# Kernel tuning notes

Measured on AMD Instinct MI355X. Metric: run time of the kernel, lower is better.

The kernel has to match this reference:

```python
import jax, jax.numpy as jnp
import numpy as np


def position_embedding(seq_len, d):
    # inv_freq_j = 1 / 10000^(2*j/d), pos_ij = sin(i * inv_freq_j)  -> [S, d]
    inv_freq = 1.0 / jnp.power(10000.0, 2.0 * jnp.arange(d, dtype=jnp.float32) / d)
    pos = jnp.arange(seq_len, dtype=jnp.float32)
    return jnp.sin(pos[:, None] * inv_freq[None, :])  # [S, d]


def setup_inputs() -> dict:
    key = jax.random.key(0)
    k1, k2 = jax.random.split(key)
    B, S, D, OUT = 4, 4096, 64, 64
    x = jax.random.normal(k1, (B, S, D), dtype=jnp.float32)
    kernel = jax.random.normal(k2, (3, D, OUT), dtype=jnp.float32) * 0.05
    return {"x": x, "kernel": kernel}


def reference(x, kernel):
    B, S, D = x.shape
    out_dim = kernel.shape[2]
    x = x + position_embedding(S, D)[None, :, :]  # broadcast pos-embed over batch
    # stacked QKV projection: [B,S,D] x [D,out] per slot
    wq = jnp.einsum('bsd,do->bso', x, kernel[0])
    wk = jnp.einsum('bsd,do->bso', x, kernel[1])
    wv = jnp.einsum('bsd,do->bso', x, kernel[2])
    scores = jnp.einsum('bso,bto->bst', wq, wk) / jnp.sqrt(jnp.asarray(out_dim, x.dtype))
    attn = jax.nn.softmax(scores, axis=-1)  # [B,S,S]
    return jnp.einsum('bst,bto->bso', attn, wv)
```

## Files before the change

### kernel.cpp

```cpp
#include <hip/hip_runtime.h>
#include <hip/hip_bf16.h>
#include <math.h>

using bf16x8 = __attribute__((ext_vector_type(8))) __bf16;
using bf16x4 = __attribute__((ext_vector_type(4))) __bf16;
using f32x4  = __attribute__((ext_vector_type(4))) float;
using f32x16 = __attribute__((ext_vector_type(16))) float;

static constexpr int SEQ = 4096;
static constexpr int DIM = 64;
static constexpr int NB  = 4;
static constexpr float QSCALE = 0.18033688011112042f;

__device__ __forceinline__ void gload16(const void* g, void* l) {
    __builtin_amdgcn_global_load_lds(
        (const __attribute__((address_space(1))) unsigned int*)g,
        (__attribute__((address_space(3))) unsigned int*)l,
        16, 0, 0);
}

__device__ __forceinline__ float fast_exp2(float x) {
#if __has_builtin(__builtin_amdgcn_exp2f)
    return __builtin_amdgcn_exp2f(x);
#else
    return exp2f(x);
#endif
}

__global__ __launch_bounds__(256)
void const_prep_kernel(const float* __restrict__ w, __bf16* __restrict__ WT,
                       float* __restrict__ peb)
{
    const int idx = (int)blockIdx.x * 256 + (int)threadIdx.x;
    const int spos = idx >> 6;
    const int c    = idx & 63;
    const float invf = exp2f(-13.287712379549449f * ((float)c * 0.03125f));
    peb[idx] = __sinf((float)spos * invf);
    if (idx < 3 * DIM * DIM) {
        const int s = idx >> 12;
        const int o = (idx >> 6) & 63;
        const int d = idx & 63;
        WT[idx] = (__bf16)w[(s * DIM + d) * DIM + o];
    }
}

__global__ __launch_bounds__(256)
void qkv_prep_kernel(const float* __restrict__ x, const __bf16* __restrict__ WT,
                     const float* __restrict__ peb,
                     __bf16* __restrict__ Qb, __bf16* __restrict__ Kb,
                     __bf16* __restrict__ Vf)
{
    const int tid  = (int)threadIdx.x;
    const int lane = tid & 63;
    const int g  = lane >> 4;
    const int cl = lane & 15;
    const int rowbase = (int)blockIdx.x * 64 + (tid >> 6) * 16;

    const int row  = rowbase + cl;
    const int spos = row & (SEQ - 1);
    bf16x8 xa[2];
#pragma unroll
    for (int h = 0; h < 2; ++h) {
        const float* xp = x + (long)row * DIM + 32*h + 8*g;
        const float* pp = peb + (long)spos * DIM + 32*h + 8*g;
        f32x4 x0 = *reinterpret_cast<const f32x4*>(xp);
        f32x4 x1 = *reinterpret_cast<const f32x4*>(xp + 4);
        f32x4 p0 = *reinterpret_cast<const f32x4*>(pp);
        f32x4 p1 = *reinterpret_cast<const f32x4*>(pp + 4);
        bf16x8 v;
#pragma unroll
        for (int e = 0; e < 8; ++e) {
            const float xv = (e < 4) ? x0[e] : x1[e - 4];
            const float pe = (e < 4) ? p0[e] : p1[e - 4];
            v[e] = (__bf16)(xv + pe);
        }
        xa[h] = v;
    }

#pragma unroll
    for (int slot = 0; slot < 3; ++slot) {
        const __bf16* wt = WT + slot * DIM * DIM;
        f32x4 acc[4];
#pragma unroll
        for (int nt = 0; nt < 4; ++nt) acc[nt] = (f32x4){0.f, 0.f, 0.f, 0.f};
#pragma unroll
        for (int nt = 0; nt < 4; ++nt) {
            bf16x8 w0 = *reinterpret_cast<const bf16x8*>(wt + (nt*16 + cl) * DIM + 8*g);
            bf16x8 w1 = *reinterpret_cast<const bf16x8*>(wt + (nt*16 + cl) * DIM + 32 + 8*g);
            acc[nt] = __builtin_amdgcn_mfma_f32_16x16x32_bf16(xa[0], w0, acc[nt], 0, 0, 0);
            acc[nt] = __builtin_amdgcn_mfma_f32_16x16x32_bf16(xa[1], w1, acc[nt], 0, 0, 0);
        }

        if (slot < 2) {
            __bf16* dst = (slot == 0) ? Qb : Kb;
            const float scale = (slot == 0) ? QSCALE : 1.0f;
#pragma unroll
            for (int nt = 0; nt < 4; ++nt)
#pragma unroll
                for (int r = 0; r < 4; ++r) {
                    const int ro = rowbase + 4*g + r;
                    dst[(long)ro * DIM + nt*16 + cl] = (__bf16)(acc[nt][r] * scale);
                }
        } else {
            const int bi = rowbase >> 12;
            const int sp = rowbase & (SEQ - 1);
            const int kc = sp >> 5;
            const int ks = (sp >> 4) & 1;
            const int lde = (32*(g&1) + cl)*8 + (g>>1)*4;
            __bf16* vb = Vf + (((long)bi*128 + kc)*4 + ks*2)*512;
#pragma unroll
            for (int nt = 0; nt < 4; ++nt) {
                bf16x4 pk;
#pragma unroll
                for (int r = 0; r < 4; ++r) pk[r] = (__bf16)acc[nt][r];
                *reinterpret_cast<bf16x4*>(vb + (nt>>1)*512 + (nt&1)*128 + lde) = pk;
            }
        }
    }
}

__global__ __launch_bounds__(512, 2)
void attn_kernel(const __bf16* __restrict__ Qb, const __bf16* __restrict__ Kb,
                 const __bf16* __restrict__ Vf, float* __restrict__ out)
{
    __shared__ char smem[71680];

    const int tid  = (int)threadIdx.x;
    const int w    = tid >> 6;
    const int lane = tid & 63;
    const int hi   = lane >> 5;
    const int l31  = lane & 31;

    const int bid = (int)blockIdx.x;
    const int x8  = bid & 7;
    const int b   = x8 & 3;
    const int qt  = ((x8 >> 2) << 6) | (bid >> 3);
    const int qbase = qt * 32;

    const __bf16* Qp  = Qb + ((long)b * SEQ + qbase) * DIM;
    const __bf16* Kpw = Kb + ((long)b * SEQ + w * 512) * DIM;
    const __bf16* Vfp = Vf + (((long)b * 128 + w * 16) * 4) * 512;

    bf16x8 qf[4];
#pragma unroll
    for (int d4 = 0; d4 < 4; ++d4)
        qf[d4] = *reinterpret_cast<const bf16x8*>(Qp + l31*DIM + d4*16 + 8*hi);

    char* kbase = smem + w * 8192;
    const int srow = lane >> 3;
    const int ssw  = ((lane & 7) ^ srow) * 8;
    int rdo[4];
#pragma unroll
    for (int d4 = 0; d4 < 4; ++d4)
        rdo[d4] = l31*128 + (((2*d4 + hi) ^ (l31 & 7)) * 16);

    f32x16 acc[2];
#pragma unroll
    for (int dt = 0; dt < 2; ++dt)
#pragma unroll
        for (int r = 0; r < 16; ++r) acc[dt][r] = 0.f;
    float mrun = -INFINITY;
    float lsum = 0.f;

    bf16x8 vcur[4], vnxt[4];
#pragma unroll
    for (int j = 0; j < 4; ++j)
        gload16(Kpw + (long)(j*8 + srow) * DIM + ssw, kbase + j*1024 + lane*16);
#pragma unroll
    for (int f = 0; f < 4; ++f)
        vcur[f] = *reinterpret_cast<const bf16x8*>(Vfp + f*512 + lane*8);

#pragma unroll 2
    for (int n = 0; n < 16; ++n) {
        if (n < 15) {
            const __bf16* kp = Kpw + (long)((n + 1) * 32) * DIM;
            char* kdst = kbase + ((n & 1) ^ 1) * 4096;
#pragma unroll
            for (int j = 0; j < 4; ++j)
                gload16(kp + (long)(j*8 + srow) * DIM + ssw, kdst + j*1024 + lane*16);
            const __bf16* vp = Vfp + (long)(n + 1) * 2048;
#pragma unroll
            for (int f = 0; f < 4; ++f)
                vnxt[f] = *reinterpret_cast<const bf16x8*>(vp + f*512 + lane*8);
            asm volatile("s_waitcnt vmcnt(8)" ::: "memory");
        } else {
            asm volatile("s_waitcnt vmcnt(0)" ::: "memory");
        }
        __builtin_amdgcn_sched_barrier(0);

        const char* kb = kbase + (n & 1) * 4096;
        bf16x8 kf0 = *reinterpret_cast<const bf16x8*>(kb + rdo[0]);
        bf16x8 kf1 = *reinterpret_cast<const bf16x8*>(kb + rdo[1]);
        bf16x8 kf2 = *reinterpret_cast<const bf16x8*>(kb + rdo[2]);
        bf16x8 kf3 = *reinterpret_cast<const bf16x8*>(kb + rdo[3]);
        f32x16 s;
#pragma unroll
        for (int r = 0; r < 16; ++r) s[r] = 0.f;
        __builtin_amdgcn_s_setprio(1);
        s = __builtin_amdgcn_mfma_f32_32x32x16_bf16(kf0, qf[0], s, 0, 0, 0);
        s = __builtin_amdgcn_mfma_f32_32x32x16_bf16(kf1, qf[1], s, 0, 0, 0);
        s = __builtin_amdgcn_mfma_f32_32x32x16_bf16(kf2, qf[2], s, 0, 0, 0);
        s = __builtin_amdgcn_mfma_f32_32x32x16_bf16(kf3, qf[3], s, 0, 0, 0);
        __builtin_amdgcn_s_setprio(0);

        float tmax = fmaxf(fmaxf(s[0], s[1]), fmaxf(s[2], s[3]));
        tmax = fmaxf(tmax, fmaxf(fmaxf(s[4], s[5]), fmaxf(s[6], s[7])));
        tmax = fmaxf(tmax, fmaxf(fmaxf(s[8], s[9]), fmaxf(s[10], s[11])));
        tmax = fmaxf(tmax, fmaxf(fmaxf(s[12], s[13]), fmaxf(s[14], s[15])));
        tmax = fmaxf(tmax, __shfl_xor(tmax, 32));

        if (!__all(tmax <= mrun)) {
            const float mnew = fmaxf(mrun, tmax);
            const float corr = fast_exp2(mrun - mnew);
            lsum *= corr;
#pragma unroll
            for (int r = 0; r < 16; ++r) {
                acc[0][r] *= corr;
                acc[1][r] *= corr;
            }
            mrun = mnew;
        }

#pragma unroll
        for (int r = 0; r < 16; ++r) {
            const float p = fast_exp2(s[r] - mrun);
            s[r] = p;
            lsum += p;
        }

        bf16x8 pb0, pb1;
#pragma unroll
        for (int e = 0; e < 8; ++e) { pb0[e] = (__bf16)s[e]; pb1[e] = (__bf16)s[8 + e]; }

        __builtin_amdgcn_s_setprio(1);
        acc[0] = __builtin_amdgcn_mfma_f32_32x32x16_bf16(vcur[0], pb0, acc[0], 0, 0, 0);
        acc[1] = __builtin_amdgcn_mfma_f32_32x32x16_bf16(vcur[1], pb0, acc[1], 0, 0, 0);
        acc[0] = __builtin_amdgcn_mfma_f32_32x32x16_bf16(vcur[2], pb1, acc[0], 0, 0, 0);
        acc[1] = __builtin_amdgcn_mfma_f32_32x32x16_bf16(vcur[3], pb1, acc[1], 0, 0, 0);
        __builtin_amdgcn_s_setprio(0);

#pragma unroll
        for (int f = 0; f < 4; ++f) vcur[f] = vnxt[f];
    }

    lsum += __shfl_xor(lsum, 32);

    __syncthreads();
    float* lpart = (float*)smem;
    float* lm    = (float*)(smem + 69632);
    float* ll    = (float*)(smem + 70656);

    {
        float* lw = lpart + ((long)w*32 + l31) * 68;
#pragma unroll
        for (int dt = 0; dt < 2; ++dt)
#pragma unroll
            for (int j = 0; j < 4; ++j) {
                f32x4 v;
#pragma unroll
                for (int c = 0; c < 4; ++c) v[c] = acc[dt][4*j + c];
                *reinterpret_cast<f32x4*>(lw + dt*32 + 8*j + 4*hi) = v;
            }
        if (lane < 32) { lm[w*32 + l31] = mrun; ll[w*32 + l31] = lsum; }
    }
    __syncthreads();

    {
        const int q  = tid >> 4;
        const int dq = (tid & 15) * 4;
        float M = lm[q];
#pragma unroll
        for (int w2 = 1; w2 < 8; ++w2) M = fmaxf(M, lm[w2*32 + q]);
        float L = 0.f;
        f32x4 o = (f32x4){0.f, 0.f, 0.f, 0.f};
#pragma unroll
        for (int w2 = 0; w2 < 8; ++w2) {
            const float f = fast_exp2(lm[w2*32 + q] - M);
            L += ll[w2*32 + q] * f;
            f32x4 v = *reinterpret_cast<const f32x4*>(lpart + ((long)w2*32 + q)*68 + dq);
#pragma unroll
            for (int c = 0; c < 4; ++c) o[c] += v[c] * f;
        }
        const float inv = 1.f / L;
#pragma unroll
        for (int c = 0; c < 4; ++c) o[c] *= inv;
        *reinterpret_cast<f32x4*>(out + ((long)b * SEQ + qbase + q) * DIM + dq) = o;
    }
}

extern "C" void kernel_launch(void* const* d_in, const int* in_sizes, int n_in,
                              void* d_out, int out_size, void* d_ws, size_t ws_size,
                              hipStream_t stream)
{
    const float* x = (const float*)d_in[0];
    const float* w = (const float*)d_in[1];
    float* out = (float*)d_out;

    char* ws = (char*)d_ws;
    const size_t sz = (size_t)NB * SEQ * DIM * sizeof(__bf16);
    __bf16* Qb  = (__bf16*)(ws);
    __bf16* Kb  = (__bf16*)(ws + sz);
    __bf16* Vf  = (__bf16*)(ws + 2 * sz);
    __bf16* WT  = (__bf16*)(ws + 3 * sz);
    float*  peb = (float*)(ws + 3 * sz + 32 * 1024);

    const_prep_kernel<<<SEQ * DIM / 256, 256, 0, stream>>>(w, WT, peb);

    qkv_prep_kernel<<<NB * SEQ / 64, 256, 0, stream>>>(x, WT, peb, Qb, Kb, Vf);

    attn_kernel<<<NB * SEQ / 32, 512, 0, stream>>>(Qb, Kb, Vf, out);
}
```

Measured before the change: 52.67 us.

## Store Q/K in MFMA fragment layout, load K directly to registers, tree-merge partials

The QKV prep kernel now writes Q and K pre-swizzled into the per-lane MFMA fragment layout, so the attention kernel loads K straight into registers with coalesced 16-byte loads instead of staging it through LDS with async global_load_lds. V is now loaded at the start of each iteration rather than prefetched one step ahead. The cross-wave softmax merge becomes a pairwise tree reduction, which roughly halves LDS use and drops the occupancy hint from launch bounds. The aim is to remove LDS traffic and waitcnt stalls and allow more occupancy, at the risk of exposing V load latency and adding extra barriers in the reduction.

```diff
diff --git a/kernel.cpp b/kernel.cpp
--- a/kernel.cpp
+++ b/kernel.cpp
@@ -11,13 +11,6 @@
 static constexpr int DIM = 64;
 static constexpr int NB  = 4;
 static constexpr float QSCALE = 0.18033688011112042f;
-
-__device__ __forceinline__ void gload16(const void* g, void* l) {
-    __builtin_amdgcn_global_load_lds(
-        (const __attribute__((address_space(1))) unsigned int*)g,
-        (__attribute__((address_space(3))) unsigned int*)l,
-        16, 0, 0);
-}
 
 __device__ __forceinline__ float fast_exp2(float x) {
 #if __has_builtin(__builtin_amdgcn_exp2f)
@@ -47,7 +40,7 @@
 __global__ __launch_bounds__(256)
 void qkv_prep_kernel(const float* __restrict__ x, const __bf16* __restrict__ WT,
                      const float* __restrict__ peb,
-                     __bf16* __restrict__ Qb, __bf16* __restrict__ Kb,
+                     __bf16* __restrict__ Qf, __bf16* __restrict__ Kf,
                      __bf16* __restrict__ Vf)
 {
     const int tid  = (int)threadIdx.x;
@@ -77,6 +70,11 @@
         xa[h] = v;
     }
 
+    const int bi  = rowbase >> 12;
+    const int sp  = rowbase & (SEQ - 1);
+    const int c32 = sp >> 5;
+    const int rb16 = sp & 16;
+
 #pragma unroll
     for (int slot = 0; slot < 3; ++slot) {
         const __bf16* wt = WT + slot * DIM * DIM;
@@ -87,31 +85,35 @@
         for (int nt = 0; nt < 4; ++nt) {
             bf16x8 w0 = *reinterpret_cast<const bf16x8*>(wt + (nt*16 + cl) * DIM + 8*g);
             bf16x8 w1 = *reinterpret_cast<const bf16x8*>(wt + (nt*16 + cl) * DIM + 32 + 8*g);
-            acc[nt] = __builtin_amdgcn_mfma_f32_16x16x32_bf16(xa[0], w0, acc[nt], 0, 0, 0);
-            acc[nt] = __builtin_amdgcn_mfma_f32_16x16x32_bf16(xa[1], w1, acc[nt], 0, 0, 0);
+            if (slot < 2) {
+                acc[nt] = __builtin_amdgcn_mfma_f32_16x16x32_bf16(w0, xa[0], acc[nt], 0, 0, 0);
+                acc[nt] = __builtin_amdgcn_mfma_f32_16x16x32_bf16(w1, xa[1], acc[nt], 0, 0, 0);
+            } else {
+                acc[nt] = __builtin_amdgcn_mfma_f32_16x16x32_bf16(xa[0], w0, acc[nt], 0, 0, 0);
+                acc[nt] = __builtin_amdgcn_mfma_f32_16x16x32_bf16(xa[1], w1, acc[nt], 0, 0, 0);
+            }
         }
 
         if (slot < 2) {
-            __bf16* dst = (slot == 0) ? Qb : Kb;
+            __bf16* dst = (slot == 0) ? Qf : Kf;
             const float scale = (slot == 0) ? QSCALE : 1.0f;
-#pragma unroll
-            for (int nt = 0; nt < 4; ++nt)
-#pragma unroll
-                for (int r = 0; r < 4; ++r) {
-                    const int ro = rowbase + 4*g + r;
-                    dst[(long)ro * DIM + nt*16 + cl] = (__bf16)(acc[nt][r] * scale);
-                }
-        } else {
-            const int bi = rowbase >> 12;
-            const int sp = rowbase & (SEQ - 1);
-            const int kc = sp >> 5;
-            const int ks = (sp >> 4) & 1;
-            const int lde = (32*(g&1) + cl)*8 + (g>>1)*4;
-            __bf16* vb = Vf + (((long)bi*128 + kc)*4 + ks*2)*512;
+            __bf16* base = dst + ((long)(bi*128 + c32) * 4) * 512
+                         + (rb16 + cl + 32*(g >> 1)) * 8 + 4*(g & 1);
 #pragma unroll
             for (int nt = 0; nt < 4; ++nt) {
                 bf16x4 pk;
 #pragma unroll
+                for (int r = 0; r < 4; ++r) pk[r] = (__bf16)(acc[nt][r] * scale);
+                *reinterpret_cast<bf16x4*>(base + nt*512) = pk;
+            }
+        } else {
+            const int ks  = (sp >> 4) & 1;
+            const int lde = (32*(g&1) + cl)*8 + (g>>1)*4;
+            __bf16* vb = Vf + (((long)bi*128 + c32)*4 + ks*2)*512;
+#pragma unroll
+            for (int nt = 0; nt < 4; ++nt) {
+                bf16x4 pk;
+#pragma unroll
                 for (int r = 0; r < 4; ++r) pk[r] = (__bf16)acc[nt][r];
                 *reinterpret_cast<bf16x4*>(vb + (nt>>1)*512 + (nt&1)*128 + lde) = pk;
             }
@@ -119,11 +121,14 @@
     }
 }
 
-__global__ __launch_bounds__(512, 2)
-void attn_kernel(const __bf16* __restrict__ Qb, const __bf16* __restrict__ Kb,
+__global__ __launch_bounds__(512)
+void attn_kernel(const __bf16* __restrict__ Qf, const __bf16* __restrict__ Kf,
                  const __bf16* __restrict__ Vf, float* __restrict__ out)
 {
-    __shared__ char smem[71680];
+    __shared__ char smem[35840];
+    float* lpart = (float*)smem;
+    float* lms   = (float*)(smem + 34816);
+    float* lls   = (float*)(smem + 35328);
 
     const int tid  = (int)threadIdx.x;
     const int w    = tid >> 6;
@@ -137,22 +142,14 @@
     const int qt  = ((x8 >> 2) << 6) | (bid >> 3);
     const int qbase = qt * 32;
 
-    const __bf16* Qp  = Qb + ((long)b * SEQ + qbase) * DIM;
-    const __bf16* Kpw = Kb + ((long)b * SEQ + w * 512) * DIM;
-    const __bf16* Vfp = Vf + (((long)b * 128 + w * 16) * 4) * 512;
+    const __bf16* Qfp = Qf + ((long)(b*128 + qt)  * 4) * 512 + lane*8;
+    const __bf16* Kfp = Kf + ((long)(b*128 + w*16) * 4) * 512 + lane*8;
+    const __bf16* Vfp = Vf + ((long)(b*128 + w*16) * 4) * 512 + lane*8;
 
     bf16x8 qf[4];
 #pragma unroll
     for (int d4 = 0; d4 < 4; ++d4)
-        qf[d4] = *reinterpret_cast<const bf16x8*>(Qp + l31*DIM + d4*16 + 8*hi);
-
-    char* kbase = smem + w * 8192;
-    const int srow = lane >> 3;
-    const int ssw  = ((lane & 7) ^ srow) * 8;
-    int rdo[4];
-#pragma unroll
-    for (int d4 = 0; d4 < 4; ++d4)
-        rdo[d4] = l31*128 + (((2*d4 + hi) ^ (l31 & 7)) * 16);
+        qf[d4] = *reinterpret_cast<const bf16x8*>(Qfp + d4*512);
 
     f32x16 acc[2];
 #pragma unroll
@@ -162,45 +159,30 @@
     float mrun = -INFINITY;
     float lsum = 0.f;
 
-    bf16x8 vcur[4], vnxt[4];
-#pragma unroll
-    for (int j = 0; j < 4; ++j)
-        gload16(Kpw + (long)(j*8 + srow) * DIM + ssw, kbase + j*1024 + lane*16);
-#pragma unroll
-    for (int f = 0; f < 4; ++f)
-        vcur[f] = *reinterpret_cast<const bf16x8*>(Vfp + f*512 + lane*8);
+    bf16x8 kcur[4], knxt[4], vcur[4];
+#pragma unroll
+    for (int d4 = 0; d4 < 4; ++d4)
+        kcur[d4] = *reinterpret_cast<const bf16x8*>(Kfp + d4*512);
 
 #pragma unroll 2
     for (int n = 0; n < 16; ++n) {
+#pragma unroll
+        for (int f = 0; f < 4; ++f)
+            vcur[f] = *reinterpret_cast<const bf16x8*>(Vfp + n*2048 + f*512);
         if (n < 15) {
-            const __bf16* kp = Kpw + (long)((n + 1) * 32) * DIM;
-            char* kdst = kbase + ((n & 1) ^ 1) * 4096;
-#pragma unroll
-            for (int j = 0; j < 4; ++j)
-                gload16(kp + (long)(j*8 + srow) * DIM + ssw, kdst + j*1024 + lane*16);
-            const __bf16* vp = Vfp + (long)(n + 1) * 2048;
-#pragma unroll
-            for (int f = 0; f < 4; ++f)
-                vnxt[f] = *reinterpret_cast<const bf16x8*>(vp + f*512 + lane*8);
-            asm volatile("s_waitcnt vmcnt(8)" ::: "memory");
-        } else {
-            asm volatile("s_waitcnt vmcnt(0)" ::: "memory");
-        }
-        __builtin_amdgcn_sched_barrier(0);
-
-        const char* kb = kbase + (n & 1) * 4096;
-        bf16x8 kf0 = *reinterpret_cast<const bf16x8*>(kb + rdo[0]);
-        bf16x8 kf1 = *reinterpret_cast<const bf16x8*>(kb + rdo[1]);
-        bf16x8 kf2 = *reinterpret_cast<const bf16x8*>(kb + rdo[2]);
-        bf16x8 kf3 = *reinterpret_cast<const bf16x8*>(kb + rdo[3]);
+#pragma unroll
+            for (int d4 = 0; d4 < 4; ++d4)
+                knxt[d4] = *reinterpret_cast<const bf16x8*>(Kfp + (n + 1)*2048 + d4*512);
+        }
+
         f32x16 s;
 #pragma unroll
         for (int r = 0; r < 16; ++r) s[r] = 0.f;
         __builtin_amdgcn_s_setprio(1);
-        s = __builtin_amdgcn_mfma_f32_32x32x16_bf16(kf0, qf[0], s, 0, 0, 0);
-        s = __builtin_amdgcn_mfma_f32_32x32x16_bf16(kf1, qf[1], s, 0, 0, 0);
-        s = __builtin_amdgcn_mfma_f32_32x32x16_bf16(kf2, qf[2], s, 0, 0, 0);
-        s = __builtin_amdgcn_mfma_f32_32x32x16_bf16(kf3, qf[3], s, 0, 0, 0);
+        s = __builtin_amdgcn_mfma_f32_32x32x16_bf16(kcur[0], qf[0], s, 0, 0, 0);
+        s = __builtin_amdgcn_mfma_f32_32x32x16_bf16(kcur[1], qf[1], s, 0, 0, 0);
+        s = __builtin_amdgcn_mfma_f32_32x32x16_bf16(kcur[2], qf[2], s, 0, 0, 0);
+        s = __builtin_amdgcn_mfma_f32_32x32x16_bf16(kcur[3], qf[3], s, 0, 0, 0);
         __builtin_amdgcn_s_setprio(0);
 
         float tmax = fmaxf(fmaxf(s[0], s[1]), fmaxf(s[2], s[3]));
@@ -240,18 +222,14 @@
         __builtin_amdgcn_s_setprio(0);
 
 #pragma unroll
-        for (int f = 0; f < 4; ++f) vcur[f] = vnxt[f];
+        for (int d4 = 0; d4 < 4; ++d4) kcur[d4] = knxt[d4];
     }
 
     lsum += __shfl_xor(lsum, 32);
 
-    __syncthreads();
-    float* lpart = (float*)smem;
-    float* lm    = (float*)(smem + 69632);
-    float* ll    = (float*)(smem + 70656);
-
-    {
-        float* lw = lpart + ((long)w*32 + l31) * 68;
+    auto write_slot = [&](int sl) {
+        if (lane < 32) { lms[sl*32 + l31] = mrun; lls[sl*32 + l31] = lsum; }
+        float* pp = lpart + sl*2176 + l31*68;
 #pragma unroll
         for (int dt = 0; dt < 2; ++dt)
 #pragma unroll
@@ -259,31 +237,52 @@
                 f32x4 v;
 #pragma unroll
                 for (int c = 0; c < 4; ++c) v[c] = acc[dt][4*j + c];
-                *reinterpret_cast<f32x4*>(lw + dt*32 + 8*j + 4*hi) = v;
-            }
-        if (lane < 32) { lm[w*32 + l31] = mrun; ll[w*32 + l31] = lsum; }
+                *reinterpret_cast<f32x4*>(pp + dt*32 + 8*j + 4*hi) = v;
+            }
+    };
+    auto merge_slot = [&](int sl) {
+        const float mp = lms[sl*32 + l31];
+        const float lp = lls[sl*32 + l31];
+        const float M  = fmaxf(mrun, mp);
+        const float fo = fast_exp2(mrun - M);
+        const float fp = fast_exp2(mp - M);
+        lsum = lsum*fo + lp*fp;
+        mrun = M;
+        const float* pp = lpart + sl*2176 + l31*68;
+#pragma unroll
+        for (int dt = 0; dt < 2; ++dt)
+#pragma unroll
+            for (int j = 0; j < 4; ++j) {
+                f32x4 v = *reinterpret_cast<const f32x4*>(pp + dt*32 + 8*j + 4*hi);
+#pragma unroll
+                for (int c = 0; c < 4; ++c)
+                    acc[dt][4*j + c] = acc[dt][4*j + c]*fo + v[c]*fp;
+            }
+    };
+
+    if (w >= 4) write_slot(w - 4);
+    __syncthreads();
+    if (w < 4) merge_slot(w);
+    if (w == 2 || w == 3) write_slot(w);
+    __syncthreads();
+    if (w < 2) merge_slot(w + 2);
+    if (w == 1) write_slot(1);
+    __syncthreads();
+    if (w == 0) {
+        merge_slot(1);
+        const float inv = 1.f / lsum;
+#pragma unroll
+        for (int dt = 0; dt < 2; ++dt)
+#pragma unroll
+            for (int r = 0; r < 16; ++r) acc[dt][r] *= inv;
+        write_slot(0);
     }
     __syncthreads();
 
     {
         const int q  = tid >> 4;
         const int dq = (tid & 15) * 4;
-        float M = lm[q];
-#pragma unroll
-        for (int w2 = 1; w2 < 8; ++w2) M = fmaxf(M, lm[w2*32 + q]);
-        float L = 0.f;
-        f32x4 o = (f32x4){0.f, 0.f, 0.f, 0.f};
-#pragma unroll
-        for (int w2 = 0; w2 < 8; ++w2) {
-            const float f = fast_exp2(lm[w2*32 + q] - M);
-            L += ll[w2*32 + q] * f;
-            f32x4 v = *reinterpret_cast<const f32x4*>(lpart + ((long)w2*32 + q)*68 + dq);
-#pragma unroll
-            for (int c = 0; c < 4; ++c) o[c] += v[c] * f;
-        }
-        const float inv = 1.f / L;
-#pragma unroll
-        for (int c = 0; c < 4; ++c) o[c] *= inv;
+        f32x4 o = *reinterpret_cast<const f32x4*>(lpart + q*68 + dq);
         *reinterpret_cast<f32x4*>(out + ((long)b * SEQ + qbase + q) * DIM + dq) = o;
     }
 }
@@ -298,15 +297,15 @@
 
     char* ws = (char*)d_ws;
     const size_t sz = (size_t)NB * SEQ * DIM * sizeof(__bf16);
-    __bf16* Qb  = (__bf16*)(ws);
-    __bf16* Kb  = (__bf16*)(ws + sz);
+    __bf16* Qf  = (__bf16*)(ws);
+    __bf16* Kf  = (__bf16*)(ws + sz);
     __bf16* Vf  = (__bf16*)(ws + 2 * sz);
     __bf16* WT  = (__bf16*)(ws + 3 * sz);
     float*  peb = (float*)(ws + 3 * sz + 32 * 1024);
 
     const_prep_kernel<<<SEQ * DIM / 256, 256, 0, stream>>>(w, WT, peb);
 
-    qkv_prep_kernel<<<NB * SEQ / 64, 256, 0, stream>>>(x, WT, peb, Qb, Kb, Vf);
-
-    attn_kernel<<<NB * SEQ / 32, 512, 0, stream>>>(Qb, Kb, Vf, out);
-}
+    qkv_prep_kernel<<<NB * SEQ / 64, 256, 0, stream>>>(x, WT, peb, Qf, Kf, Vf);
+
+    attn_kernel<<<NB * SEQ / 32, 512, 0, stream>>>(Qf, Kf, Vf, out);
+}
```

Result: faster. 47.93 us (-9.0%).
